# Kernel tuning notes

Hardware: AMD Instinct MI355X
Metric: run time of the kernel (lower is better)

## Reference

```python
import jax, jax.numpy as jnp
import numpy as np

N = 50000      # nodes
E = 800000     # edges (avg degree 16)
DIN = 128
H = 128
DOUT = 64


def setup_inputs() -> dict:
    key = jax.random.key(0)
    ks = jax.random.split(key, 8)
    x = jax.random.normal(ks[0], (N, DIN), dtype=jnp.float32)
    edge_index = jax.random.randint(ks[1], (2, E), 0, N, dtype=jnp.int32)
    def glorot(k, fi, fo):
        return jax.random.normal(k, (fi, fo), dtype=jnp.float32) * (1.0 / np.sqrt(fi))
    return {
        "x": x,
        "edge_index": edge_index,
        "W1": glorot(ks[2], DIN, H), "b1": jnp.zeros((H,), jnp.float32),
        "W2": glorot(ks[3], H, H),   "b2": jnp.zeros((H,), jnp.float32),
        "W3": glorot(ks[4], H, DOUT),"b3": jnp.zeros((DOUT,), jnp.float32),
    }


def reference(x, edge_index, W1, b1, W2, b2, W3, b3):
    n = x.shape[0]
    # GCNConv: add self-loops, symmetric degree normalization D^-1/2 (A+I) D^-1/2
    loop = jnp.arange(n, dtype=edge_index.dtype)
    src = jnp.concatenate([edge_index[0], loop])  # [E+N]
    dst = jnp.concatenate([edge_index[1], loop])
    deg = jax.ops.segment_sum(jnp.ones(src.shape, x.dtype), dst, num_segments=n)
    dinv = jnp.where(deg > 0, jax.lax.rsqrt(deg), 0.0)
    norm = dinv[src] * dinv[dst]  # [E+N]

    def conv(h, W, b):
        h = h @ W                                   # [N, out]
        msg = h[src] * norm[:, None]                # gather + scale
        return jax.ops.segment_sum(msg, dst, num_segments=n) + b

    # gelu after every layer except the last (forward breaks before act)
    h = jax.nn.gelu(conv(x, W1, b1), approximate=False)
    h = jax.nn.gelu(conv(h, W2, b2), approximate=False)
    return conv(h, W3, b3)
```

## Files before the change

kernel.cpp:

```cpp
#include <hip/hip_runtime.h>
#include <math.h>

#define NDIN 128
#define NHID 128
#define NDOUT 64

typedef _Float16 half2_t __attribute__((ext_vector_type(2)));
typedef _Float16 half4_t __attribute__((ext_vector_type(4)));
typedef _Float16 half8_t __attribute__((ext_vector_type(8)));
typedef float    float4v __attribute__((ext_vector_type(4)));

__device__ __forceinline__ float gelu_exact(float x) {
    return 0.5f * x * (1.0f + erff(x * 0.70710678118654752f));
}


__device__ void wtrans_tile(const float* __restrict__ W, _Float16* __restrict__ Wt,
                            int K, int N, int bx, int by) {
    __shared__ float tile[32][33];
    int tx = threadIdx.x & 31, ty = threadIdx.x >> 5;
    for (int i = 0; i < 32; i += 8) {
        int k = by * 32 + ty + i, nn = bx * 32 + tx;
        tile[ty + i][tx] = (k < K && nn < N) ? W[(size_t)k * N + nn] : 0.f;
    }
    __syncthreads();
    for (int i = 0; i < 32; i += 8) {
        int nn = bx * 32 + ty + i, k = by * 32 + tx;
        if (nn < N && k < K) Wt[(size_t)nn * K + k] = (_Float16)tile[tx][ty + i];
    }
}

__global__ __launch_bounds__(256) void prep0_kernel(
    const float* __restrict__ W1, _Float16* __restrict__ W1t,
    const float* __restrict__ W2, _Float16* __restrict__ W2t,
    const float* __restrict__ W3, _Float16* __restrict__ W3t,
    int* __restrict__ done) {
    int b = blockIdx.x;
    if (b < 16) {
        wtrans_tile(W1, W1t, NDIN, NHID, b & 3, b >> 2);
    } else if (b < 32) {
        wtrans_tile(W2, W2t, NHID, NHID, (b - 16) & 3, (b - 16) >> 2);
    } else if (b < 40) {
        wtrans_tile(W3, W3t, NHID, NDOUT, (b - 32) & 1, (b - 32) >> 1);
    } else {
        if (threadIdx.x < 64) done[threadIdx.x] = 0;
    }
}


template <int BN>
__device__ __forceinline__ void gemm_phaseB(
    const _Float16 (*lds_a)[136], const _Float16* __restrict__ Bt,
    _Float16* __restrict__ T, int bm, int M) {
    int tid = threadIdx.x;
    int wave = tid >> 6, lane = tid & 63;
    int m = lane & 15, quad = lane >> 4;
    const int NT = BN / 16;
    float4v acc[NT];
#pragma unroll
    for (int nt = 0; nt < NT; nt++) acc[nt] = (float4v){0.f, 0.f, 0.f, 0.f};
    int arow = (wave << 4) + m;
#pragma unroll
    for (int kc = 0; kc < 128; kc += 32) {
        half8_t a = *(const half8_t*)&lds_a[arow][kc + quad * 8];
#pragma unroll
        for (int nt = 0; nt < NT; nt++) {
            half8_t b = *(const half8_t*)&Bt[(size_t)(nt * 16 + m) * 128 + kc + quad * 8];
            acc[nt] = __builtin_amdgcn_mfma_f32_16x16x32_f16(a, b, acc[nt], 0, 0, 0);
        }
    }
#pragma unroll
    for (int nt = 0; nt < NT; nt++) {
#pragma unroll
        for (int r = 0; r < 4; r++) {
            int grow = bm + (wave << 4) + (quad << 2) + r;
            if (grow < M) T[(size_t)grow * BN + nt * 16 + m] = (_Float16)acc[nt][r];
        }
    }
}


__global__ __launch_bounds__(256) void hist_gemm1_kernel(
    const int* __restrict__ dst, int* __restrict__ hist, int E,
    const float* __restrict__ x, const _Float16* __restrict__ W1t,
    _Float16* __restrict__ T, int M, int hblocks) {
    __shared__ _Float16 lds_a[64][136];
    __shared__ int h[256];
    int b = blockIdx.x;
    int tid = threadIdx.x;
    if (b < hblocks) {
        h[tid] = 0;
        __syncthreads();
        int e = b * 256 + tid;
        if (e < E) atomicAdd(&h[dst[e] >> 8], 1);
        __syncthreads();
        hist[b * 256 + tid] = h[tid];
        return;
    }
    int bm = (b - hblocks) * 64;
#pragma unroll
    for (int j = 0; j < 8; j++) {
        int c = tid + j * 256;
        int r = c >> 5, col = (c & 31) << 2;
        int grow = bm + r;
        float4 v = make_float4(0.f, 0.f, 0.f, 0.f);
        if (grow < M) v = *(const float4*)(x + (size_t)grow * 128 + col);
        half4_t hh;
        hh[0] = (_Float16)v.x; hh[1] = (_Float16)v.y;
        hh[2] = (_Float16)v.z; hh[3] = (_Float16)v.w;
        *(half4_t*)&lds_a[r][col] = hh;
    }
    __syncthreads();
    gemm_phaseB<128>(lds_a, W1t, T, bm, M);
}


__global__ __launch_bounds__(1024) void bscan_kernel(
    int* __restrict__ hist, int* __restrict__ btotal, int* __restrict__ bbase,
    int* __restrict__ done, int EB, int nbk) {
    __shared__ int s[1024];
    __shared__ int carry;
    int b = blockIdx.x, t = threadIdx.x;
    if (t == 0) carry = 0;
    __syncthreads();
    for (int c0 = 0; c0 < EB; c0 += 1024) {
        int blk = c0 + t;
        int v = (blk < EB) ? hist[blk * 256 + b] : 0;
        s[t] = v;
        __syncthreads();
        for (int off = 1; off < 1024; off <<= 1) {
            int u = (t >= off) ? s[t - off] : 0;
            __syncthreads();
            s[t] += u;
            __syncthreads();
        }
        if (blk < EB) hist[blk * 256 + b] = carry + (s[t] - v);
        int ctot = s[1023];
        __syncthreads();
        if (t == 0) carry += ctot;
        __syncthreads();
    }
    if (t == 0) {
        atomicExch(&btotal[b], carry);
        __threadfence();
        int old = atomicAdd(&done[0], 1);
        if (old == nbk - 1) {
            int acc = 0;
            for (int i = 0; i < nbk; i++) {
                int ti = atomicAdd(&btotal[i], 0);
                bbase[i] = acc;
                acc += ti;
            }
            bbase[nbk] = acc;
        }
    }
}


__global__ __launch_bounds__(256) void scatter_kernel(
    const int* __restrict__ src, const int* __restrict__ dst,
    const int* __restrict__ hist, const int* __restrict__ bbase,
    int2* __restrict__ tmp, int E) {
    __shared__ int rank[256];
    int t = threadIdx.x;
    rank[t] = 0;
    __syncthreads();
    int blk = blockIdx.x;
    int e = blk * 256 + t;
    if (e < E) {
        int d = dst[e];
        int b = d >> 8;
        int lr = atomicAdd(&rank[b], 1);
        int pos = bbase[b] + hist[blk * 256 + b] + lr;
        tmp[pos] = make_int2(src[e], d);
    }
}


__global__ __launch_bounds__(1024) void bcsr_a_kernel(
    const int2* __restrict__ tmp, const int* __restrict__ bbase,
    int* __restrict__ rowptr, float* __restrict__ dinv, int N, int E) {
    __shared__ int cnt[256];
    __shared__ int loc[256];
    int b = blockIdx.x, t = threadIdx.x;
    if (t < 256) cnt[t] = 0;
    __syncthreads();
    int base = bbase[b], end = bbase[b + 1];
    for (int i = base + t; i < end; i += 1024)
        atomicAdd(&cnt[tmp[i].y & 255], 1);
    __syncthreads();
    if (t < 256) loc[t] = cnt[t];
    __syncthreads();
    for (int off = 1; off < 256; off <<= 1) {
        int u = (t < 256 && t >= off) ? loc[t - off] : 0;
        __syncthreads();
        if (t < 256) loc[t] += u;
        __syncthreads();
    }
    int d0 = b * 256;
    if (t < 256 && d0 + t < N) {
        rowptr[d0 + t] = base + loc[t] - cnt[t];
        dinv[d0 + t] = rsqrtf((float)(cnt[t] + 1));
    }
    if (b == 0 && t == 0) rowptr[N] = E;
}


__global__ __launch_bounds__(1024) void bcsr_b_kernel(
    const int2* __restrict__ tmp, const int* __restrict__ bbase,
    const int* __restrict__ rowptr, const float* __restrict__ dinv,
    int2* __restrict__ adj, int N) {
    __shared__ int rank[256];
    __shared__ float dloc[256];
    __shared__ int rploc[256];
    int b = blockIdx.x, t = threadIdx.x;
    int d0 = b * 256;
    if (t < 256) {
        rank[t] = 0;
        bool v = (d0 + t < N);
        dloc[t] = v ? dinv[d0 + t] : 0.f;
        rploc[t] = v ? rowptr[d0 + t] : 0;
    }
    __syncthreads();
    int base = bbase[b], end = bbase[b + 1];
    for (int i = base + t; i < end; i += 1024) {
        int2 ed = tmp[i];
        int j = ed.y & 255;
        float w = dinv[ed.x] * dloc[j];
        int r = atomicAdd(&rank[j], 1);
        adj[rploc[j] + r] = make_int2(ed.x, __float_as_int(w));
    }
}


__device__ __forceinline__ half2_t agg_node128(
    const half2_t* __restrict__ t2, const int* __restrict__ rowptr,
    const int2* __restrict__ adj, const float* __restrict__ dinv,
    const float* __restrict__ bias, int node, int lane) {
    float wself = dinv[node];
    wself *= wself;
    half2_t v = t2[(size_t)node * 64 + lane];
    float accx = wself * (float)v[0], accy = wself * (float)v[1];
    int beg = rowptr[node], end = rowptr[node + 1];
    for (int e0 = beg; e0 < end; e0 += 64) {
        int rem = end - e0;
        int j = 0; float w = 0.f;
        if (lane < rem) {
            int2 ed = adj[e0 + lane];
            j = ed.x; w = __int_as_float(ed.y);
        }
        int cnt = rem < 64 ? rem : 64;
        for (int c = 0; c < cnt; c += 16) {
#pragma unroll
            for (int i = 0; i < 16; i++) {
                int jj = __builtin_amdgcn_readlane(j, c + i);
                float ww = __int_as_float(
                    __builtin_amdgcn_readlane(__float_as_int(w), c + i));
                half2_t u = t2[(size_t)jj * 64 + lane];
                accx += ww * (float)u[0];
                accy += ww * (float)u[1];
            }
        }
    }
    float2 b = ((const float2*)bias)[lane];
    accx = gelu_exact(accx + b.x);
    accy = gelu_exact(accy + b.y);
    half2_t o; o[0] = (_Float16)accx; o[1] = (_Float16)accy;
    return o;
}


template <int BN>
__global__ __launch_bounds__(256) void agg_gemm16_kernel(
    const _Float16* __restrict__ t, const int* __restrict__ rowptr,
    const int2* __restrict__ adj, const float* __restrict__ dinv,
    const float* __restrict__ bias, const _Float16* __restrict__ Bt,
    _Float16* __restrict__ T, int M) {
    __shared__ _Float16 lds_a[16][136];
    int tid = threadIdx.x;
    int wave = tid >> 6, lane = tid & 63;
    int bm = blockIdx.x * 16;
    const half2_t* t2 = (const half2_t*)t;
#pragma unroll 1
    for (int p = 0; p < 4; p++) {
        int r = (wave << 2) + p;
        int node = bm + r;
        half2_t o;
        o[0] = (_Float16)0.f; o[1] = (_Float16)0.f;
        if (node < M) o = agg_node128(t2, rowptr, adj, dinv, bias, node, lane);
        *(half2_t*)&lds_a[r][lane << 1] = o;
    }
    __syncthreads();

    int m = lane & 15, quad = lane >> 4;
    const int NT = BN / 64;
    float4v acc[NT];
#pragma unroll
    for (int nt = 0; nt < NT; nt++) acc[nt] = (float4v){0.f, 0.f, 0.f, 0.f};
#pragma unroll
    for (int kc = 0; kc < 128; kc += 32) {
        half8_t a = *(const half8_t*)&lds_a[m][kc + quad * 8];
#pragma unroll
        for (int nt = 0; nt < NT; nt++) {
            int col = wave * (BN / 4) + nt * 16 + m;
            half8_t b = *(const half8_t*)&Bt[(size_t)col * 128 + kc + quad * 8];
            acc[nt] = __builtin_amdgcn_mfma_f32_16x16x32_f16(a, b, acc[nt], 0, 0, 0);
        }
    }
#pragma unroll
    for (int nt = 0; nt < NT; nt++) {
#pragma unroll
        for (int r = 0; r < 4; r++) {
            int grow = bm + (quad << 2) + r;
            int col = wave * (BN / 4) + nt * 16 + m;
            if (grow < M) T[(size_t)grow * BN + col] = (_Float16)acc[nt][r];
        }
    }
}


template <int F, bool DOGELU, bool OUTF16>
__global__ __launch_bounds__(256) void agg_kernel(
    const _Float16* __restrict__ t, const int* __restrict__ rowptr,
    const int2* __restrict__ adj, const float* __restrict__ dinv,
    const float* __restrict__ bias, void* __restrict__ outp, int n) {
    int node = (int)((blockIdx.x * blockDim.x + threadIdx.x) >> 6);
    int lane = threadIdx.x & 63;
    if (node >= n) return;

    float wself = dinv[node];
    wself *= wself;
    int beg = rowptr[node];
    int end = rowptr[node + 1];

    if (F == 128) {
        const half2_t* t2 = (const half2_t*)t;
        half2_t v = t2[(size_t)node * 64 + lane];
        float accx = wself * (float)v[0], accy = wself * (float)v[1];
        for (int e0 = beg; e0 < end; e0 += 64) {
            int rem = end - e0;
            int j = 0; float w = 0.f;
            if (lane < rem) {
                int2 ed = adj[e0 + lane];
                j = ed.x; w = __int_as_float(ed.y);
            }
            int cnt = rem < 64 ? rem : 64;
            for (int c = 0; c < cnt; c += 16) {
#pragma unroll
                for (int i = 0; i < 16; i++) {
                    int jj = __builtin_amdgcn_readlane(j, c + i);
                    float ww = __int_as_float(
                        __builtin_amdgcn_readlane(__float_as_int(w), c + i));
                    half2_t u = t2[(size_t)jj * 64 + lane];
                    accx += ww * (float)u[0];
                    accy += ww * (float)u[1];
                }
            }
        }
        float2 b = ((const float2*)bias)[lane];
        accx += b.x; accy += b.y;
        if (DOGELU) { accx = gelu_exact(accx); accy = gelu_exact(accy); }
        if (OUTF16) {
            half2_t o; o[0] = (_Float16)accx; o[1] = (_Float16)accy;
            ((half2_t*)outp)[(size_t)node * 64 + lane] = o;
        } else {
            float2 o; o.x = accx; o.y = accy;
            ((float2*)outp)[(size_t)node * 64 + lane] = o;
        }
    } else {
        float acc = wself * (float)t[(size_t)node * 64 + lane];
        for (int e0 = beg; e0 < end; e0 += 64) {
            int rem = end - e0;
            int j = 0; float w = 0.f;
            if (lane < rem) {
                int2 ed = adj[e0 + lane];
                j = ed.x; w = __int_as_float(ed.y);
            }
            int cnt = rem < 64 ? rem : 64;
            for (int c = 0; c < cnt; c += 16) {
#pragma unroll
                for (int i = 0; i < 16; i++) {
                    int jj = __builtin_amdgcn_readlane(j, c + i);
                    float ww = __int_as_float(
                        __builtin_amdgcn_readlane(__float_as_int(w), c + i));
                    acc += ww * (float)t[(size_t)jj * 64 + lane];
                }
            }
        }
        acc += bias[lane];
        if (DOGELU) acc = gelu_exact(acc);
        if (OUTF16) ((_Float16*)outp)[(size_t)node * 64 + lane] = (_Float16)acc;
        else        ((float*)outp)[(size_t)node * 64 + lane] = acc;
    }
}


extern "C" void kernel_launch(void* const* d_in, const int* in_sizes, int n_in,
                              void* d_out, int out_size, void* d_ws, size_t ws_size,
                              hipStream_t stream) {
    const float* x  = (const float*)d_in[0];
    const int* edge = (const int*)d_in[1];
    const float* W1 = (const float*)d_in[2];
    const float* b1 = (const float*)d_in[3];
    const float* W2 = (const float*)d_in[4];
    const float* b2 = (const float*)d_in[5];
    const float* W3 = (const float*)d_in[6];
    const float* b3 = (const float*)d_in[7];
    float* out = (float*)d_out;

    const int N = in_sizes[0] / NDIN;
    const int E = in_sizes[1] / 2;
    const int* src = edge;
    const int* dst = edge + E;
    const int NBK = (N + 255) >> 8;
    const int EB  = (E + 255) / 256;

    char* p = (char*)d_ws;
    auto alloc = [&](size_t bytes) {
        char* q = p;
        p += (bytes + 255) & ~(size_t)255;
        return q;
    };
    int*       hist     = (int*)alloc((size_t)EB * 256 * 4);
    int*       btotal   = (int*)alloc((size_t)NBK * 4);
    int*       bbase    = (int*)alloc((size_t)(NBK + 1) * 4);
    int*       done     = (int*)alloc(256);
    int*       rowptr   = (int*)alloc((size_t)(N + 1) * 4);
    float*     dinv     = (float*)alloc((size_t)N * 4);
    int2*      tmp      = (int2*)alloc((size_t)E * 8);
    int2*      adj      = (int2*)alloc((size_t)E * 8);
    _Float16*  W1t      = (_Float16*)alloc((size_t)NHID * NDIN * 2);
    _Float16*  W2t      = (_Float16*)alloc((size_t)NHID * NHID * 2);
    _Float16*  W3t      = (_Float16*)alloc((size_t)NDOUT * NHID * 2);
    _Float16*  tbuf     = (_Float16*)alloc((size_t)N * NHID * 2);
    _Float16*  hbuf     = (_Float16*)alloc((size_t)N * NHID * 2);

    dim3 blk(256);
    dim3 blk1k(1024);
    int mtiles = (N + 63) / 64;
    int ntiles16 = (N + 15) / 16;
    int agg_blocks = (N + 3) / 4;

    prep0_kernel<<<41, blk, 0, stream>>>(W1, W1t, W2, W2t, W3, W3t, done);
    hist_gemm1_kernel<<<EB + mtiles, blk, 0, stream>>>(dst, hist, E, x, W1t,
                                                       tbuf, N, EB);
    bscan_kernel<<<NBK, blk1k, 0, stream>>>(hist, btotal, bbase, done, EB, NBK);
    scatter_kernel<<<EB, blk, 0, stream>>>(src, dst, hist, bbase, tmp, E);
    bcsr_a_kernel<<<NBK, blk1k, 0, stream>>>(tmp, bbase, rowptr, dinv, N, E);
    bcsr_b_kernel<<<NBK, blk1k, 0, stream>>>(tmp, bbase, rowptr, dinv, adj, N);
    agg_gemm16_kernel<128><<<ntiles16, blk, 0, stream>>>(tbuf, rowptr, adj, dinv, b1,
                                                         W2t, hbuf, N);
    agg_gemm16_kernel<64><<<ntiles16, blk, 0, stream>>>(hbuf, rowptr, adj, dinv, b2,
                                                        W3t, tbuf, N);
    agg_kernel<64, false, false><<<agg_blocks, blk, 0, stream>>>(tbuf, rowptr, adj,
                                                                 dinv, b3, out, N);
}
```

Measured before the change: 282.4 us.

## Coarsen edge histogram and scatter into 512 fixed chunks

```diff
diff --git a/kernel.cpp b/kernel.cpp
--- a/kernel.cpp
+++ b/kernel.cpp
@@ -4,6 +4,7 @@
 #define NDIN 128
 #define NHID 128
 #define NDOUT 64
+#define CHUNKS 512
 
 typedef _Float16 half2_t __attribute__((ext_vector_type(2)));
 typedef _Float16 half4_t __attribute__((ext_vector_type(4)));
@@ -81,7 +82,7 @@
 
 
 __global__ __launch_bounds__(256) void hist_gemm1_kernel(
-    const int* __restrict__ dst, int* __restrict__ hist, int E,
+    const int* __restrict__ dst, int* __restrict__ hist, int E, int cs,
     const float* __restrict__ x, const _Float16* __restrict__ W1t,
     _Float16* __restrict__ T, int M, int hblocks) {
     __shared__ _Float16 lds_a[64][136];
@@ -91,8 +92,10 @@
     if (b < hblocks) {
         h[tid] = 0;
         __syncthreads();
-        int e = b * 256 + tid;
-        if (e < E) atomicAdd(&h[dst[e] >> 8], 1);
+        int beg = b * cs, end = beg + cs;
+        if (end > E) end = E;
+        for (int e = beg + tid; e < end; e += 256)
+            atomicAdd(&h[dst[e] >> 8], 1);
         __syncthreads();
         hist[b * 256 + tid] = h[tid];
         return;
@@ -160,19 +163,20 @@
 __global__ __launch_bounds__(256) void scatter_kernel(
     const int* __restrict__ src, const int* __restrict__ dst,
     const int* __restrict__ hist, const int* __restrict__ bbase,
-    int2* __restrict__ tmp, int E) {
+    int2* __restrict__ tmp, int E, int cs, int nbk) {
     __shared__ int rank[256];
-    int t = threadIdx.x;
+    __shared__ int base[256];
+    int c = blockIdx.x, t = threadIdx.x;
     rank[t] = 0;
-    __syncthreads();
-    int blk = blockIdx.x;
-    int e = blk * 256 + t;
-    if (e < E) {
+    base[t] = (t < nbk) ? (bbase[t] + hist[c * 256 + t]) : 0;
+    __syncthreads();
+    int beg = c * cs, end = beg + cs;
+    if (end > E) end = E;
+    for (int e = beg + t; e < end; e += 256) {
         int d = dst[e];
         int b = d >> 8;
         int lr = atomicAdd(&rank[b], 1);
-        int pos = bbase[b] + hist[blk * 256 + b] + lr;
-        tmp[pos] = make_int2(src[e], d);
+        tmp[base[b] + lr] = make_int2(src[e], d);
     }
 }
 
@@ -413,7 +417,8 @@
     const int* src = edge;
     const int* dst = edge + E;
     const int NBK = (N + 255) >> 8;
-    const int EB  = (E + 255) / 256;
+    const int CH  = CHUNKS;
+    const int CS  = (E + CH - 1) / CH;
 
     char* p = (char*)d_ws;
     auto alloc = [&](size_t bytes) {
@@ -421,9 +426,9 @@
         p += (bytes + 255) & ~(size_t)255;
         return q;
     };
-    int*       hist     = (int*)alloc((size_t)EB * 256 * 4);
+    int*       hist     = (int*)alloc((size_t)CH * 256 * 4);
     int*       btotal   = (int*)alloc((size_t)NBK * 4);
-    int*       bbase    = (int*)alloc((size_t)(NBK + 1) * 4);
+    int*       bbase    = (int*)alloc((size_t)256 * 4);
     int*       done     = (int*)alloc(256);
     int*       rowptr   = (int*)alloc((size_t)(N + 1) * 4);
     float*     dinv     = (float*)alloc((size_t)N * 4);
@@ -442,10 +447,10 @@
     int agg_blocks = (N + 3) / 4;
 
     prep0_kernel<<<41, blk, 0, stream>>>(W1, W1t, W2, W2t, W3, W3t, done);
-    hist_gemm1_kernel<<<EB + mtiles, blk, 0, stream>>>(dst, hist, E, x, W1t,
-                                                       tbuf, N, EB);
-    bscan_kernel<<<NBK, blk1k, 0, stream>>>(hist, btotal, bbase, done, EB, NBK);
-    scatter_kernel<<<EB, blk, 0, stream>>>(src, dst, hist, bbase, tmp, E);
+    hist_gemm1_kernel<<<CH + mtiles, blk, 0, stream>>>(dst, hist, E, CS, x, W1t,
+                                                       tbuf, N, CH);
+    bscan_kernel<<<NBK, blk1k, 0, stream>>>(hist, btotal, bbase, done, CH, NBK);
+    scatter_kernel<<<CH, blk, 0, stream>>>(src, dst, hist, bbase, tmp, E, CS, NBK);
     bcsr_a_kernel<<<NBK, blk1k, 0, stream>>>(tmp, bbase, rowptr, dinv, N, E);
     bcsr_b_kernel<<<NBK, blk1k, 0, stream>>>(tmp, bbase, rowptr, dinv, adj, N);
     agg_gemm16_kernel<128><<<ntiles16, blk, 0, stream>>>(tbuf, rowptr, adj, dinv, b1,
```

Measured after the change: 268.4 us. 4.9% less time.
